# Kernel optimization log

Measured on AMD Instinct MI355X. Metric: run time of the kernel, lower is better.

## Reference

```python
import jax, jax.numpy as jnp
import numpy as np

B, T, D, H, HD, C = 4, 4096, 1024, 16, 64, 64  # batch, seq, d_model, heads, head_dim, chunk
N = T // C  # T chosen as multiple of C -> pad = 0


def _dt_bias_init(k):
    u = jax.random.uniform(k, (H,), jnp.float32)
    dt = jnp.exp(u * (jnp.log(0.1) - jnp.log(0.001)) + jnp.log(0.001))
    return dt + jnp.log(-jnp.expm1(-dt))


def setup_inputs() -> dict:
    key = jax.random.key(0)
    ks = jax.random.split(key, 8)
    s = 0.02
    return {
        'out': jax.random.normal(ks[0], (B, T, D), jnp.float32),
        'w_write': jax.random.normal(ks[1], (D, D), jnp.float32) * s,   # proj_write (M=1)
        'w_gate': jax.random.normal(ks[2], (D, H), jnp.float32) * s,
        'w_out': jax.random.normal(ks[3], (D, D), jnp.float32) * s,
        'w_beta': jax.random.normal(ks[4], (D, H), jnp.float32) * s,
        'w_alpha': jax.random.normal(ks[5], (D, H), jnp.float32) * s,
        'dt_bias': _dt_bias_init(ks[6]),
        'A_log': jnp.log(jax.random.uniform(ks[7], (H,), jnp.float32, minval=0.05, maxval=4.0)),
    }


def _forward(out, w_write, w_gate, w_out, w_beta, w_alpha, dt_bias, A_log):
    x = out.astype(jnp.float32)
    d = HD
    v = (x @ w_write).reshape(B, T, H, d)                       # write values
    gate = jax.nn.sigmoid(x @ w_gate)[..., None]                # (B,T,H,1)
    beta = jax.nn.sigmoid(x @ w_beta)                           # (B,T,H)
    decay = -jnp.exp(A_log) * jax.nn.softplus(x @ w_alpha + dt_bias)  # (B,T,H), <=0

    rk = x.reshape(B, T, H, d)
    rk = rk / jnp.maximum(jnp.linalg.norm(rk, axis=-1, keepdims=True), 1e-12)  # F.normalize
    wk = jnp.pad(rk[:, :-1], ((0, 0), (1, 0), (0, 0), (0, 0)))  # token-shifted write key

    rk = rk.transpose(0, 2, 1, 3)                               # (B,H,T,d)
    wk = wk.transpose(0, 2, 1, 3)
    bet = beta.transpose(0, 2, 1)[..., None]                    # (B,H,T,1)
    v = v.transpose(0, 2, 1, 3) * bet
    wk_beta = wk * bet

    rk = rk.reshape(B, H, N, C, d)
    wk = wk.reshape(B, H, N, C, d)
    v = v.reshape(B, H, N, C, d)
    wk_beta = wk_beta.reshape(B, H, N, C, d)
    g = decay.transpose(0, 2, 1).reshape(B, H, N, C)

    cum = jnp.cumsum(g, axis=-1)                                # (B,H,N,C)
    dexp = jnp.exp(cum)[..., None]                              # (B,H,N,C,1)
    tril = jnp.tril(jnp.ones((C, C), bool))
    diff = cum[..., :, None] - cum[..., None, :]
    L = jnp.where(tril, jnp.exp(jnp.where(tril, diff, 0.0)), 0.0)  # decay kernel, lower-tri

    # WY correction: A = (I - strict_lower(-(wk_beta @ wk^T * L)))^{-1}
    kk = jnp.einsum('bhncd,bhned->bhnce', wk_beta, wk) * L
    strict_lo = jnp.tril(jnp.ones((C, C), bool), -1)
    Bm = jnp.where(strict_lo, -kk, 0.0)
    eye = jnp.eye(C, dtype=jnp.float32)
    A = jax.scipy.linalg.solve_triangular(eye - Bm, jnp.broadcast_to(eye, Bm.shape),
                                          lower=True, unit_diagonal=True)

    v_corr = A @ v                                              # (B,H,N,C,d)
    wk_cd = A @ (wk_beta * dexp)
    intra = jnp.einsum('bhncd,bhned->bhnce', rk, wk) * L        # causal intra-chunk

    def chunk_step(S, inp):
        rk_i, wk_i, vc_i, wkcd_i, intra_i, cum_i, dexp_i = inp
        v_new = vc_i - wkcd_i @ S                               # (B,H,C,d)
        o_i = (rk_i * dexp_i) @ S + intra_i @ v_new
        last = cum_i[..., -1]                                   # (B,H)
        dw = jnp.exp(last[..., None] - cum_i)[..., None]        # (B,H,C,1)
        S = S * jnp.exp(last)[..., None, None] + jnp.einsum('bhcd,bhce->bhde', wk_i * dw, v_new)
        n = jnp.sqrt(jnp.sum(S * S, axis=(-2, -1), keepdims=True))
        S = S * (jnp.minimum(n, 100.0) / jnp.maximum(n, 1e-6))  # norm clip
        return S, o_i

    xs = tuple(jnp.moveaxis(a, 2, 0) for a in (rk, wk, v_corr, wk_cd, intra, cum, dexp))
    S0 = jnp.zeros((B, H, d, d), jnp.float32)
    _, o = jax.lax.scan(chunk_step, S0, xs)                     # (N,B,H,C,d)

    o = jnp.moveaxis(o, 0, 2).reshape(B, H, T, d).transpose(0, 2, 1, 3)  # (B,T,H,d)
    o = o * gate
    return out + (o.reshape(B, T, D) @ w_out).astype(out.dtype)


def reference(out, w_write, w_gate, w_out, w_beta, w_alpha, dt_bias, A_log):
    return _forward(out, w_write, w_gate, w_out, w_beta, w_alpha, dt_bias, A_log)
```

## Files before the change

kernel.cpp:

```cpp
#include <hip/hip_runtime.h>
#include <stdint.h>

#define B_ 4
#define T_ 4096
#define D_ 1024
#define H_ 16
#define HD_ 64
#define C_ 64
#define N_ 64
#define BT_ (B_*T_)

typedef _Float16 f16;
typedef f16 f16x4 __attribute__((ext_vector_type(4)));
typedef f16 f16x8 __attribute__((ext_vector_type(8)));
typedef float f32x4 __attribute__((ext_vector_type(4)));

__device__ __forceinline__ float wave_sum(float v){
  #pragma unroll
  for(int off=32; off>0; off>>=1) v += __shfl_down(v, off);
  return __shfl(v, 0);
}

#define KSR 16
__global__ __launch_bounds__(256) void k_small(const float* __restrict__ x,
    const float* __restrict__ wg, const float* __restrict__ wb, const float* __restrict__ wa,
    const float* __restrict__ dtb, const float* __restrict__ alog,
    float* __restrict__ invn, float* __restrict__ gate, float* __restrict__ beta,
    float* __restrict__ dec){
  __shared__ float Xs [KSR][68];
  __shared__ float Wgt[H_ ][68];
  __shared__ float Wbt[H_ ][68];
  __shared__ float Wat[H_ ][68];
  int tid = threadIdx.x;
  int r = tid>>4, h = tid&15;
  int row0 = blockIdx.x*KSR;

  int sr = tid>>4, sf = (tid&15);
  int wk = tid>>2, wj = tid&3;

  float dg=0.f, db=0.f, da=0.f, ss=0.f;

  float4 px = *(const float4*)(x + (size_t)(row0+sr)*D_ + sf*4);
  float4 pg = *(const float4*)(wg + (size_t)wk*H_ + 4*wj);
  float4 pb = *(const float4*)(wb + (size_t)wk*H_ + 4*wj);
  float4 pa = *(const float4*)(wa + (size_t)wk*H_ + 4*wj);

  for(int t=0; t<16; ++t){
    __syncthreads();
    *(float4*)&Xs[sr][sf*4] = px;
    Wgt[4*wj+0][wk]=pg.x; Wgt[4*wj+1][wk]=pg.y; Wgt[4*wj+2][wk]=pg.z; Wgt[4*wj+3][wk]=pg.w;
    Wbt[4*wj+0][wk]=pb.x; Wbt[4*wj+1][wk]=pb.y; Wbt[4*wj+2][wk]=pb.z; Wbt[4*wj+3][wk]=pb.w;
    Wat[4*wj+0][wk]=pa.x; Wat[4*wj+1][wk]=pa.y; Wat[4*wj+2][wk]=pa.z; Wat[4*wj+3][wk]=pa.w;
    if(t<15){
      int k0 = (t+1)*64;
      px = *(const float4*)(x + (size_t)(row0+sr)*D_ + k0 + sf*4);
      pg = *(const float4*)(wg + (size_t)(k0+wk)*H_ + 4*wj);
      pb = *(const float4*)(wb + (size_t)(k0+wk)*H_ + 4*wj);
      pa = *(const float4*)(wa + (size_t)(k0+wk)*H_ + 4*wj);
    }
    __syncthreads();
    #pragma unroll
    for(int q=0;q<16;++q){
      float4 xv = *(const float4*)&Xs[r][4*q];
      float4 g4 = *(const float4*)&Wgt[h][4*q];
      float4 b4 = *(const float4*)&Wbt[h][4*q];
      float4 a4 = *(const float4*)&Wat[h][4*q];
      dg += xv.x*g4.x + xv.y*g4.y + xv.z*g4.z + xv.w*g4.w;
      db += xv.x*b4.x + xv.y*b4.y + xv.z*b4.z + xv.w*b4.w;
      da += xv.x*a4.x + xv.y*a4.y + xv.z*a4.z + xv.w*a4.w;
      if(t==h) ss += xv.x*xv.x + xv.y*xv.y + xv.z*xv.z + xv.w*xv.w;
    }
  }

  int o = row0*H_ + tid;
  invn[o] = 1.f/fmaxf(sqrtf(ss),1e-12f);
  gate[o] = 1.f/(1.f+expf(-dg));
  beta[o] = 1.f/(1.f+expf(-db));
  float z = da + dtb[h];
  float sp = (z>20.f)? z : log1pf(expf(z));
  dec[o] = -expf(alog[h])*sp;
}

__global__ __launch_bounds__(256) void k_tr(const float* __restrict__ w,
    f16* __restrict__ wt){
  __shared__ float T[64*68];
  int tid = threadIdx.x;
  int bj = blockIdx.x, bi = blockIdx.y;
  #pragma unroll
  for(int j=0;j<4;++j){
    int idx = tid + 256*j;
    int r = idx>>4, q = idx&15;
    float4 u = *(const float4*)(w + (size_t)(bi*64+r)*1024 + bj*64 + 4*q);
    T[(4*q+0)*68 + r] = u.x;
    T[(4*q+1)*68 + r] = u.y;
    T[(4*q+2)*68 + r] = u.z;
    T[(4*q+3)*68 + r] = u.w;
  }
  __syncthreads();
  int cc = tid>>2, seg = tid&3;
  f16 h[16];
  #pragma unroll
  for(int u2=0;u2<4;++u2){
    float4 f = *(const float4*)&T[cc*68 + seg*16 + 4*u2];
    h[4*u2+0]=(f16)f.x; h[4*u2+1]=(f16)f.y; h[4*u2+2]=(f16)f.z; h[4*u2+3]=(f16)f.w;
  }
  size_t o = (size_t)(bj*64+cc)*1024 + bi*64 + seg*16;
  *(f16x8*)(wt + o)     = *(f16x8*)&h[0];
  *(f16x8*)(wt + o + 8) = *(f16x8*)&h[8];
}

__global__ __launch_bounds__(256) void k_gemm16(const float* __restrict__ A,
    const f16* __restrict__ BT, const float* __restrict__ resid,
    float* __restrict__ C, int addres){
  __shared__ f16 Al[128*72];
  __shared__ f16 Bl[128*72];
  int tid = threadIdx.x;
  int m0 = blockIdx.y*128, n0 = blockIdx.x*128;
  int w = tid>>6, l = tid&63;
  int wm = (w>>1)*64, wn = (w&1)*64;
  int lr = l&15, lq = l>>4;
  f32x4 acc[4][4] = {};
  for(int k0=0; k0<1024; k0+=64){
    __syncthreads();
    #pragma unroll
    for(int j=0;j<8;++j){
      int idx = tid + 256*j;
      int m = idx>>4, q = idx&15;
      float4 u = *(const float4*)(A + (size_t)(m0+m)*1024 + k0 + 4*q);
      f16x4 hv; hv[0]=(f16)u.x; hv[1]=(f16)u.y; hv[2]=(f16)u.z; hv[3]=(f16)u.w;
      *(f16x4*)&Al[m*72 + 4*q] = hv;
    }
    #pragma unroll
    for(int j=0;j<4;++j){
      int idx = tid + 256*j;
      int n = idx>>3, o8 = idx&7;
      f16x8 hv = *(const f16x8*)(BT + (size_t)(n0+n)*1024 + k0 + 8*o8);
      *(f16x8*)&Bl[n*72 + 8*o8] = hv;
    }
    __syncthreads();
    #pragma unroll
    for(int kb=0; kb<64; kb+=32){
      f16x8 a[4], b[4];
      #pragma unroll
      for(int i=0;i<4;++i){
        a[i] = *(const f16x8*)&Al[(wm + i*16 + lr)*72 + kb + 8*lq];
        b[i] = *(const f16x8*)&Bl[(wn + i*16 + lr)*72 + kb + 8*lq];
      }
      #pragma unroll
      for(int mi=0;mi<4;++mi)
        #pragma unroll
        for(int ni=0;ni<4;++ni)
          acc[mi][ni] = __builtin_amdgcn_mfma_f32_16x16x32_f16(a[mi], b[ni], acc[mi][ni], 0,0,0);
    }
  }
  #pragma unroll
  for(int mi=0;mi<4;++mi){
    #pragma unroll
    for(int r=0;r<4;++r){
      int m = m0 + wm + mi*16 + lq*4 + r;
      #pragma unroll
      for(int ni=0;ni<4;++ni){
        int n = n0 + wn + ni*16 + lr;
        size_t o = (size_t)m*1024 + n;
        float v = acc[mi][ni][r];
        if(addres) v += resid[o];
        C[o] = v;
      }
    }
  }
}

__global__ __launch_bounds__(256) void k_chunk(const float* __restrict__ x,
    const float* __restrict__ invn, const float* __restrict__ beta_g,
    const float* __restrict__ dec_g, float* __restrict__ cum_g,
    float* __restrict__ vbuf, float* __restrict__ wkop,
    float* __restrict__ psum, int* __restrict__ cnt){
  int bid = blockIdx.x;
  int n = bid & 63; int h = (bid>>6) & 15; int b = bid>>10;
  int t0 = n*C_;
  __shared__ float sm[12608];
  float* WK = sm;
  float* KK = sm+4160;
  float* XW = sm+8256;
  float* BS = sm+12352;
  float* CU = sm+12416;
  float* DE = sm+12480;
  float* GS = sm+12544;
  float* XV = WK;
  int tid = threadIdx.x, w = tid>>6, l = tid&63;
  if(tid==0){ psum[bid]=0.f; cnt[bid]=0; }
  #pragma unroll
  for(int it=0; it<16; ++it){
    int idx = tid + 256*it; int c = idx>>6, dd = idx&63;
    int tw = t0+c-1;
    float wv = 0.f;
    if(tw>=0){
      size_t rr = (size_t)(b*T_+tw);
      wv = x[rr*D_ + h*64 + dd] * invn[rr*H_ + h];
    }
    WK[c*65+dd] = wv;
  }
  if(tid<64){
    size_t rr = (size_t)(b*T_+t0+tid);
    BS[tid] = beta_g[rr*H_+h];
    GS[tid] = dec_g[rr*H_+h];
  }
  __syncthreads();
  if(w==0){
    float xg = GS[l];
    #pragma unroll
    for(int off=1; off<64; off<<=1){
      float y = __shfl_up(xg, off);
      if(l>=off) xg += y;
    }
    CU[l]=xg; DE[l]=expf(xg);
    cum_g[(size_t)bid*64 + l] = xg;
  }
  __syncthreads();
  float wkj[64];
  #pragma unroll
  for(int dd=0; dd<64; ++dd) wkj[dd] = WK[l*65+dd];
  #pragma unroll 1
  for(int it=0; it<16; ++it){
    int i = w + 4*it;
    float aw=0.f;
    #pragma unroll
    for(int dd=0; dd<64; ++dd) aw += WK[i*65+dd]*wkj[dd];
    KK[i*64+l] = (l<i) ? (BS[i]*aw*expf(CU[i]-CU[l])) : 0.f;
  }
  __syncthreads();
  float rv[16], rw[16];
  #pragma unroll
  for(int it=0; it<16; ++it){
    int i = w + 4*it;
    rw[it] = WK[i*65+l]*BS[i]*DE[i];
    rv[it] = vbuf[(size_t)(b*T_+t0+i)*D_ + h*64 + l]*BS[i];
  }
  __syncthreads();
  #pragma unroll
  for(int it=0; it<16; ++it){
    int i = w + 4*it;
    XV[i*64+l] = rv[it];
    XW[i*64+l] = rw[it];
  }
  __syncthreads();
  if(w<2){
    float* Xc = (w==0) ? XV : XW;
    for(int i=1;i<64;++i){
      float acc = Xc[i*64+l];
      for(int k=0;k<i;++k) acc -= KK[i*64+k]*Xc[k*64+l];
      Xc[i*64+l] = acc;
    }
  }
  __syncthreads();
  #pragma unroll
  for(int it=0; it<16; ++it){
    int i = w + 4*it;
    vbuf[(size_t)(b*T_+t0+i)*D_ + h*64 + l] = XV[i*64+l];
    wkop[(size_t)bid*4096 + i*64 + l]       = XW[i*64+l];
  }
}

__global__ __launch_bounds__(1024, 4) void k_scan(const float* __restrict__ x,
    const float* __restrict__ invn_g, const float* __restrict__ cum_g,
    float* __restrict__ vbuf, float* __restrict__ wkop,
    float* __restrict__ psum, int* __restrict__ cnt){
  int bh = blockIdx.x & 63, cg = blockIdx.x >> 6;
  int b = bh>>4, h = bh&15, col0 = cg*16;
  __shared__ float sm[15448];
  float* WCD = sm;
  float* RK  = sm+4352;
  float* WKT = sm+8704;
  float* VNS = sm+13056;
  float* ST  = sm+14144;
  float* DW  = sm+15232;
  float* DEc = sm+15296;
  float* PREV= sm+15360;
  float* P   = sm+15424;
  float* NRM = sm+15440;
  int tid = threadIdx.x, w = tid>>6, l = tid&63;
  int c = tid>>4, q4 = tid&15;
  int col = tid&15;

  for(int i=tid;i<1088;i+=1024) ST[i]=0.f;
  if(tid<64) PREV[tid]=0.f;

  float4 pW, pR; float pIv, pV, pC=0.f, pLast=0.f;
  {
    size_t base0 = (size_t)bh*N_*4096;
    pW = *(const float4*)(wkop + base0 + (size_t)tid*4);
    pR = *(const float4*)(x + (size_t)(b*T_+c)*D_ + h*64 + 4*q4);
    pIv = invn_g[(size_t)(b*T_+c)*H_ + h];
    pV  = vbuf[(size_t)(b*T_+c)*D_ + h*64 + col0+col];
    if(tid<64){
      pC    = cum_g[(size_t)bh*N_*64 + tid];
      pLast = cum_g[(size_t)bh*N_*64 + 63];
    }
  }
  __syncthreads();

  float scale = 1.f;
  for(int n=0;n<N_;++n){
    int t0 = n*C_;
    size_t base = ((size_t)bh*N_+n)*4096;
    *(float4*)&WCD[c*68+4*q4] = pW;
    float4 rv4;
    rv4.x=pR.x*pIv; rv4.y=pR.y*pIv; rv4.z=pR.z*pIv; rv4.w=pR.w*pIv;
    *(float4*)&RK[c*68+4*q4] = rv4;
    if(c<63){
      WKT[(4*q4+0)*68 + c+1]=rv4.x;
      WKT[(4*q4+1)*68 + c+1]=rv4.y;
      WKT[(4*q4+2)*68 + c+1]=rv4.z;
      WKT[(4*q4+3)*68 + c+1]=rv4.w;
    }
    if(tid<64){
      WKT[tid*68+0] = PREV[tid];
      DW[tid]  = expf(pLast-pC);
      DEc[tid] = expf(pC);
    }
    if(n>0 && tid==0){
      int slot = bh*N_ + n-1;
      int guard = 0;
      while(__hip_atomic_load(&cnt[slot], __ATOMIC_ACQUIRE, __HIP_MEMORY_SCOPE_AGENT) < 4
            && guard < (1<<20)){
        __builtin_amdgcn_s_sleep(8);
        ++guard;
      }
      NRM[0] = __hip_atomic_load(&psum[slot], __ATOMIC_RELAXED, __HIP_MEMORY_SCOPE_AGENT);
    }
    __syncthreads();
    if(n>0){
      float nr = sqrtf(NRM[0]);
      scale = fminf(nr,100.f)/fmaxf(nr,1e-6f);
    }
    float vcur = pV;
    if(n+1<N_){
      int t1 = t0 + C_;
      size_t base1 = base + 4096;
      pW = *(const float4*)(wkop + base1 + (size_t)tid*4);
      pR = *(const float4*)(x + (size_t)(b*T_+t1+c)*D_ + h*64 + 4*q4);
      pIv = invn_g[(size_t)(b*T_+t1+c)*H_ + h];
      pV  = vbuf[(size_t)(b*T_+t1+c)*D_ + h*64 + col0+col];
      if(tid<64){
        pC    = cum_g[((size_t)bh*N_+n+1)*64 + tid];
        pLast = cum_g[((size_t)bh*N_+n+1)*64 + 63];
      }
    }
    float da=0.f, dro=0.f;
    #pragma unroll
    for(int q=0;q<16;++q){
      float4 wv = *(const float4*)&WCD[c*68+4*q];
      float4 rr = *(const float4*)&RK [c*68+4*q];
      float4 sv = *(const float4*)&ST [col*68+4*q];
      da  += wv.x*sv.x+wv.y*sv.y+wv.z*sv.z+wv.w*sv.w;
      dro += rr.x*sv.x+rr.y*sv.y+rr.z*sv.z+rr.w*sv.w;
    }
    float vn = vcur - scale*da;
    vbuf[(size_t)(b*T_+t0+c)*D_ + h*64 + col0+col] = vn;
    wkop[base + c*64 + col0+col] = DEc[c]*scale*dro;
    VNS[col*68+c] = vn*DW[c];
    __syncthreads();
    if(tid<64) PREV[tid] = RK[63*68+tid];
    float sold = ST[col*68+c];
    float sn = DEc[63]*scale*sold;
    #pragma unroll
    for(int q=0;q<16;++q){
      float4 wt = *(const float4*)&WKT[c*68+4*q];
      float4 vt = *(const float4*)&VNS[col*68+4*q];
      sn += wt.x*vt.x+wt.y*vt.y+wt.z*vt.z+wt.w*vt.w;
    }
    float p = sn*sn;
    p = wave_sum(p);
    if(l==0) P[w]=p;
    __syncthreads();
    if(tid==0 && n+1<N_){
      float pl=0.f;
      #pragma unroll
      for(int i=0;i<16;++i) pl += P[i];
      int slot = bh*N_ + n;
      __hip_atomic_fetch_add(&psum[slot], pl, __ATOMIC_RELAXED, __HIP_MEMORY_SCOPE_AGENT);
      __hip_atomic_fetch_add(&cnt[slot], 1, __ATOMIC_RELEASE, __HIP_MEMORY_SCOPE_AGENT);
    }
    ST[col*68+c] = sn;
  }
}

__global__ __launch_bounds__(256) void k_o(const float* __restrict__ x,
    const float* __restrict__ invn, const float* __restrict__ cum_g,
    const float* __restrict__ wkop, const float* __restrict__ gate_g,
    float* __restrict__ vbuf){
  int bid = blockIdx.x; int n = bid&63, h=(bid>>6)&15, b=bid>>10;
  int t0 = n*C_;
  __shared__ float sm[8256];
  float* RK = sm;
  float* VN = sm+4096;
  float* CU = sm+8192;
  float* INT = RK;
  int tid=threadIdx.x, w=tid>>6, l=tid&63;
  if(tid<64) CU[tid] = cum_g[(size_t)bid*64 + tid];
  #pragma unroll 1
  for(int it=0;it<16;++it){
    int idx = tid+256*it; int c=idx>>6, dd=idx&63;
    size_t rr = (size_t)(b*T_+t0+c);
    RK[c*64+dd] = x[rr*D_ + h*64 + dd] * invn[rr*H_ + h];
    VN[idx]     = vbuf[rr*D_ + h*64 + dd];
  }
  __syncthreads();
  float wkj[64];
  {
    int tw = t0+l-1;
    if(tw>=0){
      size_t r2 = (size_t)(b*T_+tw);
      float iv = invn[r2*H_ + h];
      #pragma unroll
      for(int d4=0; d4<16; ++d4){
        float4 u = *(const float4*)(x + r2*D_ + h*64 + 4*d4);
        wkj[4*d4+0]=u.x*iv; wkj[4*d4+1]=u.y*iv;
        wkj[4*d4+2]=u.z*iv; wkj[4*d4+3]=u.w*iv;
      }
    } else {
      #pragma unroll
      for(int dd=0;dd<64;++dd) wkj[dd]=0.f;
    }
  }
  #pragma unroll 1
  for(int it=0;it<16;++it){
    int i = w + 4*it;
    float ar = 0.f;
    #pragma unroll
    for(int d4=0; d4<16; ++d4){
      float4 r4 = *(const float4*)&RK[i*64 + 4*d4];
      ar += r4.x*wkj[4*d4] + r4.y*wkj[4*d4+1] + r4.z*wkj[4*d4+2] + r4.w*wkj[4*d4+3];
    }
    float val = (l<=i) ? (ar*expf(CU[i]-CU[l])) : 0.f;
    INT[i*64+l] = val;
  }
  __syncthreads();
  float vn_col[64];
  #pragma unroll
  for(int k=0;k<64;++k) vn_col[k] = VN[k*64+l];
  #pragma unroll 1
  for(int it=0;it<16;++it){
    int c = w+4*it;
    float acc = 0.f;
    #pragma unroll
    for(int d4=0; d4<16; ++d4){
      float4 i4 = *(const float4*)&INT[c*64 + 4*d4];
      acc += i4.x*vn_col[4*d4] + i4.y*vn_col[4*d4+1] + i4.z*vn_col[4*d4+2] + i4.w*vn_col[4*d4+3];
    }
    size_t rr = (size_t)(b*T_+t0+c);
    float g  = gate_g[rr*H_ + h];
    float op = wkop[(size_t)bid*4096 + c*64 + l];
    vbuf[rr*D_ + h*64 + l] = (op + acc)*g;
  }
}

extern "C" void kernel_launch(void* const* d_in, const int* in_sizes, int n_in,
                              void* d_out, int out_size, void* d_ws, size_t ws_size,
                              hipStream_t stream) {
  const float* x       = (const float*)d_in[0];
  const float* w_write = (const float*)d_in[1];
  const float* w_gate  = (const float*)d_in[2];
  const float* w_out   = (const float*)d_in[3];
  const float* w_beta  = (const float*)d_in[4];
  const float* w_alpha = (const float*)d_in[5];
  const float* dt_bias = (const float*)d_in[6];
  const float* A_log   = (const float*)d_in[7];
  float* outp = (float*)d_out;

  const size_t big   = (size_t)BT_*D_;
  const size_t small = (size_t)BT_*H_;
  const size_t nslot = (size_t)B_*H_*N_;
  const size_t wsz   = (size_t)D_*D_;
  const size_t need  = (2*big + 5*small + 2*nslot)*sizeof(float) + 2*wsz*sizeof(f16);
  if(ws_size < need) return;

  float* ws   = (float*)d_ws;
  float* vbuf = ws;
  float* wkop = vbuf + big;
  float* invn = wkop + big;
  float* gate = invn + small;
  float* beta = gate + small;
  float* dec  = beta + small;
  float* cum  = dec  + small;
  float* psum = cum  + small;
  int*   cnt  = (int*)(psum + nslot);
  f16*   wtw  = (f16*)(cnt + nslot);
  f16*   wto  = wtw + wsz;

  k_tr<<<dim3(16,16), dim3(256), 0, stream>>>(w_write, wtw);
  k_tr<<<dim3(16,16), dim3(256), 0, stream>>>(w_out,  wto);
  k_small<<<dim3(BT_/KSR), dim3(256), 0, stream>>>(x, w_gate, w_beta, w_alpha,
      dt_bias, A_log, invn, gate, beta, dec);
  k_gemm16<<<dim3(D_/128, BT_/128), dim3(256), 0, stream>>>(x, wtw,
      (const float*)0, vbuf, 0);
  k_chunk<<<dim3(B_*H_*N_), dim3(256), 0, stream>>>(x, invn, beta, dec,
      cum, vbuf, wkop, psum, cnt);
  k_scan<<<dim3(4*B_*H_), dim3(1024), 0, stream>>>(x, invn, cum, vbuf, wkop,
      psum, cnt);
  k_o<<<dim3(B_*H_*N_), dim3(256), 0, stream>>>(x, invn, cum, wkop, gate, vbuf);
  k_gemm16<<<dim3(D_/128, BT_/128), dim3(256), 0, stream>>>(vbuf, wto, x,
      outp, 1);
}
```

Measured before the change: 1.249 ms.

## Register-block scan over four columns, merge transposes, swizzle GEMM block order

```diff
diff --git a/kernel.cpp b/kernel.cpp
--- a/kernel.cpp
+++ b/kernel.cpp
@@ -19,6 +19,9 @@
   #pragma unroll
   for(int off=32; off>0; off>>=1) v += __shfl_down(v, off);
   return __shfl(v, 0);
+}
+__device__ __forceinline__ float dot4(float4 a, float4 b){
+  return a.x*b.x + a.y*b.y + a.z*b.z + a.w*b.w;
 }
 
 #define KSR 16
@@ -65,10 +68,10 @@
       float4 g4 = *(const float4*)&Wgt[h][4*q];
       float4 b4 = *(const float4*)&Wbt[h][4*q];
       float4 a4 = *(const float4*)&Wat[h][4*q];
-      dg += xv.x*g4.x + xv.y*g4.y + xv.z*g4.z + xv.w*g4.w;
-      db += xv.x*b4.x + xv.y*b4.y + xv.z*b4.z + xv.w*b4.w;
-      da += xv.x*a4.x + xv.y*a4.y + xv.z*a4.z + xv.w*a4.w;
-      if(t==h) ss += xv.x*xv.x + xv.y*xv.y + xv.z*xv.z + xv.w*xv.w;
+      dg += dot4(xv,g4);
+      db += dot4(xv,b4);
+      da += dot4(xv,a4);
+      if(t==h) ss += dot4(xv,xv);
     }
   }
 
@@ -81,8 +84,10 @@
   dec[o] = -expf(alog[h])*sp;
 }
 
-__global__ __launch_bounds__(256) void k_tr(const float* __restrict__ w,
-    f16* __restrict__ wt){
+__global__ __launch_bounds__(256) void k_tr(const float* __restrict__ w0,
+    const float* __restrict__ w1, f16* __restrict__ t0, f16* __restrict__ t1){
+  const float* w = blockIdx.z ? w1 : w0;
+  f16* wt        = blockIdx.z ? t1 : t0;
   __shared__ float T[64*68];
   int tid = threadIdx.x;
   int bj = blockIdx.x, bi = blockIdx.y;
@@ -115,7 +120,9 @@
   __shared__ f16 Al[128*72];
   __shared__ f16 Bl[128*72];
   int tid = threadIdx.x;
-  int m0 = blockIdx.y*128, n0 = blockIdx.x*128;
+  int bid = blockIdx.x;
+  int g = bid>>6, t = bid&63;
+  int m0 = (g*8 + (t&7))*128, n0 = (t>>3)*128;
   int w = tid>>6, l = tid&63;
   int wm = (w>>1)*64, wn = (w&1)*64;
   int lr = l&15, lq = l>>4;
@@ -265,8 +272,8 @@
     const float* __restrict__ invn_g, const float* __restrict__ cum_g,
     float* __restrict__ vbuf, float* __restrict__ wkop,
     float* __restrict__ psum, int* __restrict__ cnt){
-  int bh = blockIdx.x & 63, cg = blockIdx.x >> 6;
-  int b = bh>>4, h = bh&15, col0 = cg*16;
+  int bh = blockIdx.x & 63, cg4 = blockIdx.x >> 6;
+  int b = bh>>4, h = bh&15, col0 = cg4*16;
   __shared__ float sm[15448];
   float* WCD = sm;
   float* RK  = sm+4352;
@@ -279,19 +286,20 @@
   float* P   = sm+15424;
   float* NRM = sm+15440;
   int tid = threadIdx.x, w = tid>>6, l = tid&63;
-  int c = tid>>4, q4 = tid&15;
-  int col = tid&15;
+  int cs = tid>>4, q4 = tid&15;
+  int gc = tid>>2, cq = tid&3;
 
   for(int i=tid;i<1088;i+=1024) ST[i]=0.f;
   if(tid<64) PREV[tid]=0.f;
 
-  float4 pW, pR; float pIv, pV, pC=0.f, pLast=0.f;
+  float4 pW, pR, pV; float pIv, pC=0.f, pLast=0.f;
   {
     size_t base0 = (size_t)bh*N_*4096;
     pW = *(const float4*)(wkop + base0 + (size_t)tid*4);
-    pR = *(const float4*)(x + (size_t)(b*T_+c)*D_ + h*64 + 4*q4);
-    pIv = invn_g[(size_t)(b*T_+c)*H_ + h];
-    pV  = vbuf[(size_t)(b*T_+c)*D_ + h*64 + col0+col];
+    pR = *(const float4*)(x + (size_t)(b*T_+cs)*D_ + h*64 + 4*q4);
+    pIv = invn_g[(size_t)(b*T_+cs)*H_ + h];
+    if(tid<256)
+      pV = *(const float4*)(vbuf + (size_t)(b*T_+gc)*D_ + h*64 + col0 + 4*cq);
     if(tid<64){
       pC    = cum_g[(size_t)bh*N_*64 + tid];
       pLast = cum_g[(size_t)bh*N_*64 + 63];
@@ -303,15 +311,15 @@
   for(int n=0;n<N_;++n){
     int t0 = n*C_;
     size_t base = ((size_t)bh*N_+n)*4096;
-    *(float4*)&WCD[c*68+4*q4] = pW;
+    *(float4*)&WCD[cs*68+4*q4] = pW;
     float4 rv4;
     rv4.x=pR.x*pIv; rv4.y=pR.y*pIv; rv4.z=pR.z*pIv; rv4.w=pR.w*pIv;
-    *(float4*)&RK[c*68+4*q4] = rv4;
-    if(c<63){
-      WKT[(4*q4+0)*68 + c+1]=rv4.x;
-      WKT[(4*q4+1)*68 + c+1]=rv4.y;
-      WKT[(4*q4+2)*68 + c+1]=rv4.z;
-      WKT[(4*q4+3)*68 + c+1]=rv4.w;
+    *(float4*)&RK[cs*68+4*q4] = rv4;
+    if(cs<63){
+      WKT[(4*q4+0)*68 + cs+1]=rv4.x;
+      WKT[(4*q4+1)*68 + cs+1]=rv4.y;
+      WKT[(4*q4+2)*68 + cs+1]=rv4.z;
+      WKT[(4*q4+3)*68 + cs+1]=rv4.w;
     }
     if(tid<64){
       WKT[tid*68+0] = PREV[tid];
@@ -333,55 +341,85 @@
       float nr = sqrtf(NRM[0]);
       scale = fminf(nr,100.f)/fmaxf(nr,1e-6f);
     }
-    float vcur = pV;
+    float4 vcur;
+    if(tid<256) vcur = pV;
     if(n+1<N_){
       int t1 = t0 + C_;
       size_t base1 = base + 4096;
       pW = *(const float4*)(wkop + base1 + (size_t)tid*4);
-      pR = *(const float4*)(x + (size_t)(b*T_+t1+c)*D_ + h*64 + 4*q4);
-      pIv = invn_g[(size_t)(b*T_+t1+c)*H_ + h];
-      pV  = vbuf[(size_t)(b*T_+t1+c)*D_ + h*64 + col0+col];
+      pR = *(const float4*)(x + (size_t)(b*T_+t1+cs)*D_ + h*64 + 4*q4);
+      pIv = invn_g[(size_t)(b*T_+t1+cs)*H_ + h];
+      if(tid<256)
+        pV = *(const float4*)(vbuf + (size_t)(b*T_+t1+gc)*D_ + h*64 + col0 + 4*cq);
       if(tid<64){
         pC    = cum_g[((size_t)bh*N_+n+1)*64 + tid];
         pLast = cum_g[((size_t)bh*N_+n+1)*64 + 63];
       }
     }
-    float da=0.f, dro=0.f;
-    #pragma unroll
-    for(int q=0;q<16;++q){
-      float4 wv = *(const float4*)&WCD[c*68+4*q];
-      float4 rr = *(const float4*)&RK [c*68+4*q];
-      float4 sv = *(const float4*)&ST [col*68+4*q];
-      da  += wv.x*sv.x+wv.y*sv.y+wv.z*sv.z+wv.w*sv.w;
-      dro += rr.x*sv.x+rr.y*sv.y+rr.z*sv.z+rr.w*sv.w;
-    }
-    float vn = vcur - scale*da;
-    vbuf[(size_t)(b*T_+t0+c)*D_ + h*64 + col0+col] = vn;
-    wkop[base + c*64 + col0+col] = DEc[c]*scale*dro;
-    VNS[col*68+c] = vn*DW[c];
+    if(tid<256){
+      float4 da = {0.f,0.f,0.f,0.f}, dr = {0.f,0.f,0.f,0.f};
+      #pragma unroll
+      for(int q=0;q<16;++q){
+        float4 wv = *(const float4*)&WCD[gc*68+4*q];
+        float4 rr = *(const float4*)&RK [gc*68+4*q];
+        float4 s0 = *(const float4*)&ST [(4*cq+0)*68+4*q];
+        float4 s1 = *(const float4*)&ST [(4*cq+1)*68+4*q];
+        float4 s2 = *(const float4*)&ST [(4*cq+2)*68+4*q];
+        float4 s3 = *(const float4*)&ST [(4*cq+3)*68+4*q];
+        da.x += dot4(wv,s0); da.y += dot4(wv,s1);
+        da.z += dot4(wv,s2); da.w += dot4(wv,s3);
+        dr.x += dot4(rr,s0); dr.y += dot4(rr,s1);
+        dr.z += dot4(rr,s2); dr.w += dot4(rr,s3);
+      }
+      float dwc = DW[gc], dsc = DEc[gc]*scale;
+      float4 vn;
+      vn.x = vcur.x - scale*da.x; vn.y = vcur.y - scale*da.y;
+      vn.z = vcur.z - scale*da.z; vn.w = vcur.w - scale*da.w;
+      *(float4*)(vbuf + (size_t)(b*T_+t0+gc)*D_ + h*64 + col0 + 4*cq) = vn;
+      float4 op;
+      op.x = dsc*dr.x; op.y = dsc*dr.y; op.z = dsc*dr.z; op.w = dsc*dr.w;
+      *(float4*)(wkop + base + gc*64 + col0 + 4*cq) = op;
+      VNS[(4*cq+0)*68+gc] = vn.x*dwc;
+      VNS[(4*cq+1)*68+gc] = vn.y*dwc;
+      VNS[(4*cq+2)*68+gc] = vn.z*dwc;
+      VNS[(4*cq+3)*68+gc] = vn.w*dwc;
+    }
     __syncthreads();
     if(tid<64) PREV[tid] = RK[63*68+tid];
-    float sold = ST[col*68+c];
-    float sn = DEc[63]*scale*sold;
-    #pragma unroll
-    for(int q=0;q<16;++q){
-      float4 wt = *(const float4*)&WKT[c*68+4*q];
-      float4 vt = *(const float4*)&VNS[col*68+4*q];
-      sn += wt.x*vt.x+wt.y*vt.y+wt.z*vt.z+wt.w*vt.w;
-    }
-    float p = sn*sn;
-    p = wave_sum(p);
-    if(l==0) P[w]=p;
+    float sn0=0.f, sn1=0.f, sn2=0.f, sn3=0.f;
+    if(tid<256){
+      float el = DEc[63]*scale;
+      sn0 = el*ST[(4*cq+0)*68+gc];
+      sn1 = el*ST[(4*cq+1)*68+gc];
+      sn2 = el*ST[(4*cq+2)*68+gc];
+      sn3 = el*ST[(4*cq+3)*68+gc];
+      #pragma unroll
+      for(int q=0;q<16;++q){
+        float4 wt = *(const float4*)&WKT[gc*68+4*q];
+        float4 v0 = *(const float4*)&VNS[(4*cq+0)*68+4*q];
+        float4 v1 = *(const float4*)&VNS[(4*cq+1)*68+4*q];
+        float4 v2 = *(const float4*)&VNS[(4*cq+2)*68+4*q];
+        float4 v3 = *(const float4*)&VNS[(4*cq+3)*68+4*q];
+        sn0 += dot4(wt,v0); sn1 += dot4(wt,v1);
+        sn2 += dot4(wt,v2); sn3 += dot4(wt,v3);
+      }
+      float p = sn0*sn0 + sn1*sn1 + sn2*sn2 + sn3*sn3;
+      p = wave_sum(p);
+      if(l==0) P[w]=p;
+    }
     __syncthreads();
     if(tid==0 && n+1<N_){
-      float pl=0.f;
-      #pragma unroll
-      for(int i=0;i<16;++i) pl += P[i];
+      float pl = P[0]+P[1]+P[2]+P[3];
       int slot = bh*N_ + n;
       __hip_atomic_fetch_add(&psum[slot], pl, __ATOMIC_RELAXED, __HIP_MEMORY_SCOPE_AGENT);
       __hip_atomic_fetch_add(&cnt[slot], 1, __ATOMIC_RELEASE, __HIP_MEMORY_SCOPE_AGENT);
     }
-    ST[col*68+c] = sn;
+    if(tid<256){
+      ST[(4*cq+0)*68+gc] = sn0;
+      ST[(4*cq+1)*68+gc] = sn1;
+      ST[(4*cq+2)*68+gc] = sn2;
+      ST[(4*cq+3)*68+gc] = sn3;
+    }
   }
 }
 
@@ -488,17 +526,16 @@
   f16*   wtw  = (f16*)(cnt + nslot);
   f16*   wto  = wtw + wsz;
 
-  k_tr<<<dim3(16,16), dim3(256), 0, stream>>>(w_write, wtw);
-  k_tr<<<dim3(16,16), dim3(256), 0, stream>>>(w_out,  wto);
+  k_tr<<<dim3(16,16,2), dim3(256), 0, stream>>>(w_write, w_out, wtw, wto);
   k_small<<<dim3(BT_/KSR), dim3(256), 0, stream>>>(x, w_gate, w_beta, w_alpha,
       dt_bias, A_log, invn, gate, beta, dec);
-  k_gemm16<<<dim3(D_/128, BT_/128), dim3(256), 0, stream>>>(x, wtw,
+  k_gemm16<<<dim3(1024), dim3(256), 0, stream>>>(x, wtw,
       (const float*)0, vbuf, 0);
   k_chunk<<<dim3(B_*H_*N_), dim3(256), 0, stream>>>(x, invn, beta, dec,
       cum, vbuf, wkop, psum, cnt);
   k_scan<<<dim3(4*B_*H_), dim3(1024), 0, stream>>>(x, invn, cum, vbuf, wkop,
       psum, cnt);
   k_o<<<dim3(B_*H_*N_), dim3(256), 0, stream>>>(x, invn, cum, wkop, gate, vbuf);
-  k_gemm16<<<dim3(D_/128, BT_/128), dim3(256), 0, stream>>>(vbuf, wto, x,
+  k_gemm16<<<dim3(1024), dim3(256), 0, stream>>>(vbuf, wto, x,
       outp, 1);
 }
```

Result: slower. 1.914 ms (+53.2%).
